# Kernel optimization log

Hardware: AMD Instinct MI355X
Metric: run time of the kernel (lower is better)

## Reference

```python
import jax, jax.numpy as jnp
import numpy as np

N_AGENTS = 16      # args['num_agents']
BATCH = 8192       # args['n_rollout_threads'] -> number of independent graphs
OBS = 64           # cent_obs_shape[0] // n_nodes
HID = 128          # args['hidden_sizes'][0]
N_LAYERS = 2       # args['n_layers']
USE_RES = True     # args['use_res']


def _build_edges():
    # complete graph (no self loops) per graph, block-diagonal over BATCH graphs
    i, j = np.meshgrid(np.arange(N_AGENTS), np.arange(N_AGENTS), indexing='ij')
    m = i != j
    bs, bd = i[m], j[m]                      # [240]
    off = (np.arange(BATCH) * N_AGENTS)[:, None]
    src = (bs[None, :] + off).ravel().astype(np.int32)  # [BATCH*240]
    dst = (bd[None, :] + off).ravel().astype(np.int32)
    return src, dst


def setup_inputs() -> dict:
    key = jax.random.key(0)
    ks = jax.random.split(key, 5)
    N = BATCH * N_AGENTS
    src, dst = _build_edges()
    return {
        'cent_obs': jax.random.normal(ks[0], (N, OBS), jnp.float32),
        'w_emb': jax.random.normal(ks[1], (OBS, HID), jnp.float32) / np.sqrt(OBS).astype(np.float32),
        'b_emb': jnp.zeros((HID,), jnp.float32),
        'w_gcn': jax.random.normal(ks[2], (N_LAYERS, HID, HID), jnp.float32) / np.sqrt(HID).astype(np.float32),
        'b_gcn': jnp.zeros((N_LAYERS, HID), jnp.float32),
        'w_fc1': jax.random.normal(ks[3], (HID, 1), jnp.float32) / np.sqrt(HID).astype(np.float32),
        'b_fc1': jnp.zeros((1,), jnp.float32),
        'edge_src': jnp.asarray(src),
        'edge_dst': jnp.asarray(dst),
    }


def reference(cent_obs, w_emb, b_emb, w_gcn, b_gcn, w_fc1, b_fc1, edge_src, edge_dst):
    N = cent_obs.shape[0]
    # embedding_in
    x = cent_obs @ w_emb + b_emb                           # [N, HID]
    # GCNConv normalization with added self-loops (PyG default, sym norm)
    loop = jnp.arange(N, dtype=edge_src.dtype)
    src = jnp.concatenate([edge_src, loop])
    dst = jnp.concatenate([edge_dst, loop])
    deg = jax.ops.segment_sum(jnp.ones_like(dst, dtype=x.dtype), dst, num_segments=N)
    inv_sqrt = jax.lax.rsqrt(deg)
    norm = (inv_sqrt[src] * inv_sqrt[dst])[:, None]        # [E+N, 1]
    for l in range(N_LAYERS):
        h = x @ w_gcn[l]                                   # linear transform
        agg = jax.ops.segment_sum(h[src] * norm, dst, num_segments=N) + b_gcn[l]
        x = jnp.tanh(agg + x if USE_RES else agg)
    value = x @ w_fc1 + b_fc1                              # [N, 1]
    value = value.reshape(BATCH, -1)                       # [BATCH, n_nodes]
    return value.mean(axis=1).reshape(-1, 1)               # [BATCH, 1]
```

## Files before the change

### kernel.cpp

```cpp
#include <hip/hip_runtime.h>


#define N_GRAPHS 8192
#define BLOCK    256
#define NBLOCKS  (N_GRAPHS / 8)

typedef __attribute__((ext_vector_type(8)))  short short8;
typedef __attribute__((ext_vector_type(4)))  float floatx4;
typedef __attribute__((ext_vector_type(16))) float floatx16;

#define MFMA16(a, b, c) __builtin_amdgcn_mfma_f32_16x16x32_bf16((a), (b), (c), 0, 0, 0)
#define MFMA32(a, b, c) __builtin_amdgcn_mfma_f32_32x32x16_bf16((a), (b), (c), 0, 0, 0)

#define EMB_LO   1024
#define GCN_BASE 2048
#define GCN_LO   2048

union fragu { unsigned int u[4]; short8 s8; };

__device__ __forceinline__ unsigned fbits(float x) {
  union { float f; unsigned u; } v; v.f = x; return v.u;
}
__device__ __forceinline__ float bitsf(unsigned u) {
  union { float f; unsigned u; } v; v.u = u; return v.f;
}
__device__ __forceinline__ void bsplit(float x, short& hi, short& lo) {
  unsigned hb = fbits(x) & 0xFFFF0000u;
  hi = (short)(hb >> 16);
  lo = (short)(fbits(x - bitsf(hb)) >> 16);
}
__device__ __forceinline__ unsigned hpack(unsigned b_odd, unsigned b_even) {
  return __builtin_amdgcn_perm(b_odd, b_even, 0x07060302u);
}
__device__ __forceinline__ void mk_frags(float4 a, float4 b, short8& hi, short8& lo) {
  fragu H, L;
  H.u[0] = hpack(fbits(a.y), fbits(a.x));
  H.u[1] = hpack(fbits(a.w), fbits(a.z));
  H.u[2] = hpack(fbits(b.y), fbits(b.x));
  H.u[3] = hpack(fbits(b.w), fbits(b.z));
  float l0 = a.x - bitsf(fbits(a.x) & 0xFFFF0000u);
  float l1 = a.y - bitsf(fbits(a.y) & 0xFFFF0000u);
  float l2 = a.z - bitsf(fbits(a.z) & 0xFFFF0000u);
  float l3 = a.w - bitsf(fbits(a.w) & 0xFFFF0000u);
  float l4 = b.x - bitsf(fbits(b.x) & 0xFFFF0000u);
  float l5 = b.y - bitsf(fbits(b.y) & 0xFFFF0000u);
  float l6 = b.z - bitsf(fbits(b.z) & 0xFFFF0000u);
  float l7 = b.w - bitsf(fbits(b.w) & 0xFFFF0000u);
  L.u[0] = hpack(fbits(l1), fbits(l0));
  L.u[1] = hpack(fbits(l3), fbits(l2));
  L.u[2] = hpack(fbits(l5), fbits(l4));
  L.u[3] = hpack(fbits(l7), fbits(l6));
  hi = H.s8; lo = L.s8;
}
__device__ __forceinline__ float fast_tanh(float z) {
  float e = __expf(2.0f * z);
  return 1.0f - __fdividef(2.0f, e + 1.0f);
}

__global__ __launch_bounds__(BLOCK) void gcn_prep(
    const float* __restrict__ w_emb, const float* __restrict__ w_gcn,
    unsigned short* __restrict__ wsS)
{
  int idx = blockIdx.x * BLOCK + threadIdx.x;
  if (idx >= 40960) return;
  int f = idx >> 3, j = idx & 7;
  const float* src;
  int hi_f, lo_f;
  if (f < 1024) {
    int ks = f >> 8, t = (f >> 6) & 3, L = f & 63;
    int k0 = ks * 16 + (L >> 5) * 8;
    int n  = t * 32 + (L & 31);
    src = w_emb + k0 * 128 + n;
    hi_f = f; lo_f = f + EMB_LO;
  } else {
    int f2 = f - 1024;
    int l = f2 >> 11, r = f2 & 2047;
    int kc = r >> 9, nt = (r >> 6) & 7, L = r & 63;
    int k0 = kc * 32 + (L >> 4) * 8;
    int n  = nt * 16 + (L & 15);
    src = w_gcn + l * 16384 + k0 * 128 + n;
    hi_f = GCN_BASE + l * 4096 + r; lo_f = hi_f + GCN_LO;
  }
  short h, l_;
  bsplit(src[j * 128], h, l_);
  wsS[hi_f * 8 + j] = (unsigned short)h;
  wsS[lo_f * 8 + j] = (unsigned short)l_;
}

__global__ __launch_bounds__(BLOCK, 4) void gcn_main(
    const float* __restrict__ obs,
    const float* __restrict__ b_emb,
    const float* __restrict__ b_gcn,
    const float* __restrict__ w_fc1,
    const float* __restrict__ b_fc1,
    const short8* __restrict__ tab,
    float* __restrict__ out)
{
  __shared__ short sA[2 * 4 * 16 * 40];
  __shared__ float sH[8][129];

  const int tid = threadIdx.x;
  const int w   = tid >> 6;
  const int L   = tid & 63;
  const int m32 = L & 31;
  const int kh  = L >> 5;
  const int c16 = L & 15;
  const int q   = L >> 4;
  const int gw  = blockIdx.x * 8 + 2 * w;

  {
    unsigned int* za = (unsigned int*)sA;
    #pragma unroll
    for (int jz = 0; jz < 5; ++jz) {
      int i   = tid + 256 * jz;
      int tb_ = i / 160;
      int rm  = i - tb_ * 160;
      int rr  = rm / 20, cw = rm - rr * 20;
      za[tb_ * 320 + (rr + 8) * 20 + cw] = 0;
    }
  }

  const float* op = obs + (gw * 16 + m32) * 64 + kh * 8;
  float4 oa0 = *(const float4*)(op);
  float4 oa1 = *(const float4*)(op + 4);
  float4 ob0 = *(const float4*)(op + 16);
  float4 ob1 = *(const float4*)(op + 20);

  floatx16 x[4];
  #pragma unroll
  for (int t = 0; t < 4; ++t) {
    float b = b_emb[t * 32 + m32];
    #pragma unroll
    for (int r = 0; r < 16; ++r) x[t][r] = b;
  }

  #pragma unroll
  for (int s = 0; s < 4; ++s) {
    short8 ah, al;
    mk_frags(oa0, oa1, ah, al);
    oa0 = ob0; oa1 = ob1;
    if (s < 2) {
      ob0 = *(const float4*)(op + (s + 2) * 16);
      ob1 = *(const float4*)(op + (s + 2) * 16 + 4);
    }
    #pragma unroll
    for (int t = 0; t < 4; ++t) {
      int idx = (s * 4 + t) * 64 + L;
      short8 bh = tab[idx];
      short8 bl = tab[idx + EMB_LO];
      x[t] = MFMA32(ah, bh, x[t]);
      x[t] = MFMA32(al, bh, x[t]);
      x[t] = MFMA32(ah, bl, x[t]);
    }
  }

  #pragma unroll 1
  for (int l = 0; l < 2; ++l) {
    const short8* t0 = tab + GCN_BASE + l * 4096 + (2 * w) * 64 + L;
    const short8* t1 = t0 + 64;
    short8 cbh0 = t0[0], cbh1 = t1[0];
    short8 cbl0 = t0[GCN_LO], cbl1 = t1[GCN_LO];

    #pragma unroll
    for (int t = 0; t < 4; ++t) {
      float s0 = x[t][0], s1 = x[t][8];
      #pragma unroll
      for (int r = 1; r < 8; ++r) { s0 += x[t][r]; s1 += x[t][r + 8]; }
      s0 += __shfl_xor(s0, 32);
      s1 += __shfl_xor(s1, 32);
      s0 *= 0.0625f; s1 *= 0.0625f;
      #pragma unroll
      for (int rr = 0; rr < 2; ++rr) {
        float v = rr ? s1 : s0;
        unsigned hb = fbits(v) & 0xFFFF0000u;
        unsigned vb = (kh == 0) ? hb : fbits(v - bitsf(hb));
        unsigned nb = (unsigned)__shfl_xor((int)vb, 1);
        unsigned pw = hpack(nb, vb);
        if ((m32 & 1) == 0) {
          int si = kh * 2560 + t * 640 + (2 * w + rr) * 40
                 + (m32 >> 3) * 8 + (m32 & 7);
          *(unsigned int*)&sA[si] = pw;
        }
      }
    }
    __syncthreads();

    floatx4 h0 = {0.f, 0.f, 0.f, 0.f};
    floatx4 h1 = {0.f, 0.f, 0.f, 0.f};
    #pragma unroll
    for (int kc = 0; kc < 4; ++kc) {
      short8 ah = *(const short8*)&sA[kc * 640 + c16 * 40 + q * 8];
      short8 al = *(const short8*)&sA[2560 + kc * 640 + c16 * 40 + q * 8];
      short8 nbh0, nbh1, nbl0, nbl1;
      if (kc < 3) {
        nbh0 = t0[(kc + 1) * 512];
        nbh1 = t1[(kc + 1) * 512];
        nbl0 = t0[(kc + 1) * 512 + GCN_LO];
        nbl1 = t1[(kc + 1) * 512 + GCN_LO];
      }
      h0 = MFMA16(ah, cbh0, h0); h1 = MFMA16(ah, cbh1, h1);
      h0 = MFMA16(al, cbh0, h0); h1 = MFMA16(al, cbh1, h1);
      h0 = MFMA16(ah, cbl0, h0); h1 = MFMA16(ah, cbl1, h1);
      cbh0 = nbh0; cbh1 = nbh1; cbl0 = nbl0; cbl1 = nbl1;
    }
    if (q < 2) {
      #pragma unroll
      for (int r = 0; r < 4; ++r) {
        sH[q * 4 + r][(2 * w) * 16 + c16]     = h0[r];
        sH[q * 4 + r][(2 * w + 1) * 16 + c16] = h1[r];
      }
    }
    __syncthreads();

    #pragma unroll
    for (int t = 0; t < 4; ++t) {
      float b  = b_gcn[l * 128 + t * 32 + m32];
      float zA = sH[2 * w][t * 32 + m32] + b;
      float zB = sH[2 * w + 1][t * 32 + m32] + b;
      #pragma unroll
      for (int r = 0; r < 8; ++r) {
        x[t][r]     = fast_tanh(x[t][r] + zA);
        x[t][r + 8] = fast_tanh(x[t][r + 8] + zB);
      }
    }
  }

  float vA = 0.f, vB = 0.f;
  #pragma unroll
  for (int t = 0; t < 4; ++t) {
    float wf = w_fc1[t * 32 + m32];
    float sA_ = 0.f, sB_ = 0.f;
    #pragma unroll
    for (int r = 0; r < 8; ++r) { sA_ += x[t][r]; sB_ += x[t][r + 8]; }
    vA = fmaf(sA_, wf, vA);
    vB = fmaf(sB_, wf, vB);
  }
  #pragma unroll
  for (int d = 32; d >= 1; d >>= 1) {
    vA += __shfl_xor(vA, d);
    vB += __shfl_xor(vB, d);
  }
  if (L == 0) {
    float bf = b_fc1[0];
    out[gw]     = vA * 0.0625f + bf;
    out[gw + 1] = vB * 0.0625f + bf;
  }
}

extern "C" void kernel_launch(void* const* d_in, const int* in_sizes, int n_in,
                              void* d_out, int out_size, void* d_ws, size_t ws_size,
                              hipStream_t stream) {
  const float* obs    = (const float*)d_in[0];
  const float* w_emb  = (const float*)d_in[1];
  const float* b_emb  = (const float*)d_in[2];
  const float* w_gcn  = (const float*)d_in[3];
  const float* b_gcn  = (const float*)d_in[4];
  const float* w_fc1  = (const float*)d_in[5];
  const float* b_fc1  = (const float*)d_in[6];
  float* out = (float*)d_out;

  gcn_prep<<<160, BLOCK, 0, stream>>>(w_emb, w_gcn, (unsigned short*)d_ws);
  gcn_main<<<NBLOCKS, BLOCK, 0, stream>>>(obs, b_emb, b_gcn, w_fc1, b_fc1,
                                          (const short8*)d_ws, out);
}
```

Before: 119.7 us.

## Double block to 16 graphs, stage embedding weights in LDS, fill full MFMA rows

Blocks grow to 512 threads and 16 graphs. The embedding weight fragments are copied once per block into shared memory and read from there, so they are no longer fetched from global memory by every wave. The GCN mean-pooled A tile now holds 16 graph rows with no zero padding, and each wave computes one 16-column output tile instead of two. This removes the zeroing pass and halves wasted MFMA rows. It costs 32KB of extra LDS per block, which may lower occupancy, and adds a block-wide sync after the weight staging.

```diff
diff --git a/kernel.cpp b/kernel.cpp
--- a/kernel.cpp
+++ b/kernel.cpp
@@ -2,8 +2,9 @@
 
 
 #define N_GRAPHS 8192
-#define BLOCK    256
-#define NBLOCKS  (N_GRAPHS / 8)
+#define BLOCK    512
+#define GPB      16
+#define NBLOCKS  (N_GRAPHS / GPB)
 
 typedef __attribute__((ext_vector_type(8)))  short short8;
 typedef __attribute__((ext_vector_type(4)))  float floatx4;
@@ -57,11 +58,11 @@
   return 1.0f - __fdividef(2.0f, e + 1.0f);
 }
 
-__global__ __launch_bounds__(BLOCK) void gcn_prep(
+__global__ __launch_bounds__(256) void gcn_prep(
     const float* __restrict__ w_emb, const float* __restrict__ w_gcn,
     unsigned short* __restrict__ wsS)
 {
-  int idx = blockIdx.x * BLOCK + threadIdx.x;
+  int idx = blockIdx.x * 256 + threadIdx.x;
   if (idx >= 40960) return;
   int f = idx >> 3, j = idx & 7;
   const float* src;
@@ -96,8 +97,9 @@
     const short8* __restrict__ tab,
     float* __restrict__ out)
 {
-  __shared__ short sA[2 * 4 * 16 * 40];
-  __shared__ float sH[8][129];
+  __shared__ short8 sEmb[2048];
+  __shared__ short  sA[2 * 4 * 16 * 40];
+  __shared__ float  sH[16][132];
 
   const int tid = threadIdx.x;
   const int w   = tid >> 6;
@@ -106,19 +108,7 @@
   const int kh  = L >> 5;
   const int c16 = L & 15;
   const int q   = L >> 4;
-  const int gw  = blockIdx.x * 8 + 2 * w;
-
-  {
-    unsigned int* za = (unsigned int*)sA;
-    #pragma unroll
-    for (int jz = 0; jz < 5; ++jz) {
-      int i   = tid + 256 * jz;
-      int tb_ = i / 160;
-      int rm  = i - tb_ * 160;
-      int rr  = rm / 20, cw = rm - rr * 20;
-      za[tb_ * 320 + (rr + 8) * 20 + cw] = 0;
-    }
-  }
+  const int gw  = blockIdx.x * GPB + 2 * w;
 
   const float* op = obs + (gw * 16 + m32) * 64 + kh * 8;
   float4 oa0 = *(const float4*)(op);
@@ -126,6 +116,9 @@
   float4 ob0 = *(const float4*)(op + 16);
   float4 ob1 = *(const float4*)(op + 20);
 
+  #pragma unroll
+  for (int i = 0; i < 4; ++i) sEmb[i * BLOCK + tid] = tab[i * BLOCK + tid];
+
   floatx16 x[4];
   #pragma unroll
   for (int t = 0; t < 4; ++t) {
@@ -133,6 +126,7 @@
     #pragma unroll
     for (int r = 0; r < 16; ++r) x[t][r] = b;
   }
+  __syncthreads();
 
   #pragma unroll
   for (int s = 0; s < 4; ++s) {
@@ -146,8 +140,8 @@
     #pragma unroll
     for (int t = 0; t < 4; ++t) {
       int idx = (s * 4 + t) * 64 + L;
-      short8 bh = tab[idx];
-      short8 bl = tab[idx + EMB_LO];
+      short8 bh = sEmb[idx];
+      short8 bl = sEmb[idx + EMB_LO];
       x[t] = MFMA32(ah, bh, x[t]);
       x[t] = MFMA32(al, bh, x[t]);
       x[t] = MFMA32(ah, bl, x[t]);
@@ -156,10 +150,13 @@
 
   #pragma unroll 1
   for (int l = 0; l < 2; ++l) {
-    const short8* t0 = tab + GCN_BASE + l * 4096 + (2 * w) * 64 + L;
-    const short8* t1 = t0 + 64;
-    short8 cbh0 = t0[0], cbh1 = t1[0];
-    short8 cbl0 = t0[GCN_LO], cbl1 = t1[GCN_LO];
+    const short8* tbase = tab + GCN_BASE + l * 4096 + w * 64 + L;
+    short8 bh[4], bl[4];
+    #pragma unroll
+    for (int kc = 0; kc < 4; ++kc) {
+      bh[kc] = tbase[kc * 512];
+      bl[kc] = tbase[kc * 512 + GCN_LO];
+    }
 
     #pragma unroll
     for (int t = 0; t < 4; ++t) {
@@ -177,39 +174,25 @@
         unsigned nb = (unsigned)__shfl_xor((int)vb, 1);
         unsigned pw = hpack(nb, vb);
         if ((m32 & 1) == 0) {
-          int si = kh * 2560 + t * 640 + (2 * w + rr) * 40
-                 + (m32 >> 3) * 8 + (m32 & 7);
+          int si = kh * 2560 + t * 640 + (2 * w + rr) * 40 + m32;
           *(unsigned int*)&sA[si] = pw;
         }
       }
     }
     __syncthreads();
 
-    floatx4 h0 = {0.f, 0.f, 0.f, 0.f};
-    floatx4 h1 = {0.f, 0.f, 0.f, 0.f};
+    floatx4 h = {0.f, 0.f, 0.f, 0.f};
     #pragma unroll
     for (int kc = 0; kc < 4; ++kc) {
       short8 ah = *(const short8*)&sA[kc * 640 + c16 * 40 + q * 8];
       short8 al = *(const short8*)&sA[2560 + kc * 640 + c16 * 40 + q * 8];
-      short8 nbh0, nbh1, nbl0, nbl1;
-      if (kc < 3) {
-        nbh0 = t0[(kc + 1) * 512];
-        nbh1 = t1[(kc + 1) * 512];
-        nbl0 = t0[(kc + 1) * 512 + GCN_LO];
-        nbl1 = t1[(kc + 1) * 512 + GCN_LO];
-      }
-      h0 = MFMA16(ah, cbh0, h0); h1 = MFMA16(ah, cbh1, h1);
-      h0 = MFMA16(al, cbh0, h0); h1 = MFMA16(al, cbh1, h1);
-      h0 = MFMA16(ah, cbl0, h0); h1 = MFMA16(ah, cbl1, h1);
-      cbh0 = nbh0; cbh1 = nbh1; cbl0 = nbl0; cbl1 = nbl1;
-    }
-    if (q < 2) {
-      #pragma unroll
-      for (int r = 0; r < 4; ++r) {
-        sH[q * 4 + r][(2 * w) * 16 + c16]     = h0[r];
-        sH[q * 4 + r][(2 * w + 1) * 16 + c16] = h1[r];
-      }
-    }
+      h = MFMA16(ah, bh[kc], h);
+      h = MFMA16(al, bh[kc], h);
+      h = MFMA16(ah, bl[kc], h);
+    }
+    #pragma unroll
+    for (int r = 0; r < 4; ++r)
+      sH[q * 4 + r][w * 16 + c16] = h[r];
     __syncthreads();
 
     #pragma unroll
@@ -259,7 +242,7 @@
   const float* b_fc1  = (const float*)d_in[6];
   float* out = (float*)d_out;
 
-  gcn_prep<<<160, BLOCK, 0, stream>>>(w_emb, w_gcn, (unsigned short*)d_ws);
+  gcn_prep<<<160, 256, 0, stream>>>(w_emb, w_gcn, (unsigned short*)d_ws);
   gcn_main<<<NBLOCKS, BLOCK, 0, stream>>>(obs, b_emb, b_gcn, w_fc1, b_fc1,
                                           (const short8*)d_ws, out);
 }
```

Result: no change. 120.3 us (+0.5%).
